# Kernel optimization log

Hardware: AMD Instinct MI355X
Metric: run time of the kernel (lower is better)

The kernel has to match this reference:

```python
import jax, jax.numpy as jnp
import numpy as np

EMB = 1024
HEADS = 16

def setup_inputs() -> dict:
    key = jax.random.key(0)
    ks = jax.random.split(key, 9)
    s = 1.0 / np.sqrt(EMB)
    x = jax.random.normal(ks[0], (2, 2048, EMB), dtype=jnp.float32)
    Wq = jax.random.normal(ks[1], (EMB, EMB), dtype=jnp.float32) * s
    bq = jax.random.normal(ks[2], (EMB,), dtype=jnp.float32) * s
    Wk = jax.random.normal(ks[3], (EMB, EMB), dtype=jnp.float32) * s
    bk = jax.random.normal(ks[4], (EMB,), dtype=jnp.float32) * s
    Wv = jax.random.normal(ks[5], (EMB, EMB), dtype=jnp.float32) * s
    bv = jax.random.normal(ks[6], (EMB,), dtype=jnp.float32) * s
    Wo = jax.random.normal(ks[7], (EMB, EMB), dtype=jnp.float32) * s
    bo = jax.random.normal(ks[8], (EMB,), dtype=jnp.float32) * s
    return {"x": x, "Wq": Wq, "bq": bq, "Wk": Wk, "bk": bk, "Wv": Wv, "bv": bv, "Wo": Wo, "bo": bo}

def reference(x, Wq, bq, Wk, bk, Wv, bv, Wo, bo):
    B, N, E = x.shape
    H = HEADS
    D = E // H
    # q/k/v projections, split heads: b n (h d) -> b h n d
    def proj(W, b):
        y = jnp.einsum('bne,ef->bnf', x, W.T) + b
        return y.reshape(B, N, H, D).transpose(0, 2, 1, 3)
    q = proj(Wq, bq)
    k = proj(Wk, bk)
    v = proj(Wv, bv)
    energy = jnp.einsum('bhqd,bhkd->bhqk', q, k)
    scaling = jnp.asarray(E, x.dtype) ** 0.5  # note: sqrt(emb_size), as in source
    att = jax.nn.softmax(energy / scaling, axis=-1)
    out = jnp.einsum('bhqk,bhkd->bhqd', att, v)
    out = out.transpose(0, 2, 1, 3).reshape(B, N, E)  # b h n d -> b n (h d)
    return jnp.einsum('bne,ef->bnf', out, Wo.T) + bo
```

## Files before the change

### kernel.cpp

```cpp
#include <hip/hip_runtime.h>
#include <hip/hip_bf16.h>
#include <stdint.h>

typedef __bf16 bf16;
typedef __bf16 bf16x8 __attribute__((ext_vector_type(8)));
typedef __bf16 bf16x4 __attribute__((ext_vector_type(4)));
typedef __bf16 bf16x2 __attribute__((ext_vector_type(2)));
typedef float  f32x4  __attribute__((ext_vector_type(4)));
typedef float  f32x16 __attribute__((ext_vector_type(16)));
typedef unsigned int uint;

#define MFMA(a,b,c)   __builtin_amdgcn_mfma_f32_16x16x32_bf16((a),(b),(c),0,0,0)
#define MFMA32(a,b,c) __builtin_amdgcn_mfma_f32_32x32x16_bf16((a),(b),(c),0,0,0)
#define EXP2(x)       __builtin_amdgcn_exp2f(x)

__device__ __forceinline__ void gload_lds16(const void* g, void* lds) {
  __builtin_amdgcn_global_load_lds(
      (const __attribute__((address_space(1))) uint32_t*)g,
      (__attribute__((address_space(3))) uint32_t*)lds, 16, 0, 0);
}

__device__ __forceinline__ uint pk_bf16(float lo, float hi) {
  bf16x2 v; v[0] = (bf16)lo; v[1] = (bf16)hi;
  return __builtin_bit_cast(uint, v);
}

__global__ __launch_bounds__(256) void k_cvt(
    const float* __restrict__ x,
    const float* __restrict__ wq, const float* __restrict__ wk,
    const float* __restrict__ wv, const float* __restrict__ wo,
    bf16* __restrict__ xb, bf16* __restrict__ wqb, bf16* __restrict__ wkb,
    bf16* __restrict__ wvb, bf16* __restrict__ wob)
{
  int r = blockIdx.y;
  const float* s; bf16* d; int n;
  switch (r) {
    case 0: s = x;  d = xb;  n = 4194304; break;
    case 1: s = wq; d = wqb; n = 1048576; break;
    case 2: s = wk; d = wkb; n = 1048576; break;
    case 3: s = wv; d = wvb; n = 1048576; break;
    default: s = wo; d = wob; n = 1048576; break;
  }
  int i = (blockIdx.x * 256 + threadIdx.x) * 8;
  if (i >= n) return;
  const float4* sp = (const float4*)(s + i);
  float4 a = sp[0], b = sp[1];
  bf16x8 o;
  o[0]=(bf16)a.x; o[1]=(bf16)a.y; o[2]=(bf16)a.z; o[3]=(bf16)a.w;
  o[4]=(bf16)b.x; o[5]=(bf16)b.y; o[6]=(bf16)b.z; o[7]=(bf16)b.w;
  *(bf16x8*)(d + i) = o;
}

__global__ __launch_bounds__(256, 2) void k_gemm_qkv(
    const bf16* __restrict__ A,
    const bf16* __restrict__ Wq, const bf16* __restrict__ Wk, const bf16* __restrict__ Wv,
    const float* __restrict__ bq, const float* __restrict__ bk, const float* __restrict__ bv,
    bf16* __restrict__ Qw, bf16* __restrict__ Kw, bf16* __restrict__ Vtw)
{
  __shared__ __align__(16) char As[2][8192];
  __shared__ __align__(16) char Bs[2][8192];
  int tid = threadIdx.x;
  int wv4 = tid >> 6, l = tid & 63, lo = l & 15, hi = l >> 4;
  int f = blockIdx.y * 32 + blockIdx.x;
  int xcd = f & 7, i8 = f >> 3;
  int mt = xcd * 4 + (i8 & 3);
  int ft = i8 >> 2;
  int wsel = ft >> 3;
  const bf16* W = (wsel == 0) ? Wq : (wsel == 1) ? Wk : Wv;
  const float* bias = (wsel == 0) ? bq : (wsel == 1) ? bk : bv;
  int f0 = (ft & 7) * 128;
  const bf16* Ab = A + (size_t)mt * 128 * 1024;
  const bf16* Wb = W + (size_t)f0 * 1024;
  const bf16* Pa = (wsel < 2) ? Wb : Ab;
  const bf16* Pb = (wsel < 2) ? Ab : Wb;
  int wm = wv4 >> 1, wf = wv4 & 1;
  f32x4 acc[4][4];
  #pragma unroll
  for (int i = 0; i < 4; i++)
    #pragma unroll
    for (int j = 0; j < 4; j++) acc[i][j] = (f32x4){0.f, 0.f, 0.f, 0.f};

  #define STAGEG(t, bi) {                                              \
    int k0 = (t) * 32;                                                 \
    _Pragma("unroll")                                                  \
    for (int p = 0; p < 2; p++) {                                      \
      int sp = p * 256 + tid;                                          \
      int row = sp >> 2, s = sp & 3;                                   \
      int gc = k0 + 8 * (s ^ ((row >> 1) & 3));                        \
      gload_lds16(Pa + (size_t)row * 1024 + gc, As[bi] + sp * 16);     \
      gload_lds16(Pb + (size_t)row * 1024 + gc, Bs[bi] + sp * 16);     \
    } }

  STAGEG(0, 0);
  for (int t = 0; t < 32; ++t) {
    __syncthreads();
    if (t < 31) STAGEG(t + 1, (t + 1) & 1);
    const char* Ac = As[t & 1];
    const char* Bc = Bs[t & 1];
    bf16x8 af[4], bfr[4];
    #pragma unroll
    for (int ms = 0; ms < 4; ms++) {
      int row = wm * 64 + ms * 16 + lo;
      af[ms] = *(const bf16x8*)(Ac + row * 64 + 16 * (hi ^ ((row >> 1) & 3)));
    }
    #pragma unroll
    for (int fs = 0; fs < 4; fs++) {
      int row = wf * 64 + fs * 16 + lo;
      bfr[fs] = *(const bf16x8*)(Bc + row * 64 + 16 * (hi ^ ((row >> 1) & 3)));
    }
    __builtin_amdgcn_s_setprio(1);
    #pragma unroll
    for (int ms = 0; ms < 4; ms++)
      #pragma unroll
      for (int fs = 0; fs < 4; fs++)
        acc[ms][fs] = MFMA(af[ms], bfr[fs], acc[ms][fs]);
    __builtin_amdgcn_s_setprio(0);
  }
  #undef STAGEG

  if (wsel < 2) {
    bf16* Outp = (wsel == 0) ? Qw : Kw;
    float qs = (wsel == 0) ? 0.0450842199527801f : 1.0f;
    #pragma unroll
    for (int ms = 0; ms < 4; ms++) {
      int fl = f0 + wm * 64 + ms * 16 + hi * 4;
      int h = fl >> 6, dd = fl & 63;
      float4 b4 = *(const float4*)(bias + fl);
      #pragma unroll
      for (int fs = 0; fs < 4; fs++) {
        int m = mt * 128 + wf * 64 + fs * 16 + lo;
        int b = m >> 11, nn = m & 2047;
        bf16x4 w;
        #pragma unroll
        for (int r = 0; r < 4; r++)
          w[r] = (bf16)((acc[ms][fs][r] + ((const float*)&b4)[r]) * qs);
        *(bf16x4*)(Outp + (((size_t)(b * 16 + h) * 2048 + nn) * 64) + dd) = w;
      }
    }
  } else {
    #pragma unroll
    for (int fs = 0; fs < 4; fs++) {
      int fl = f0 + wf * 64 + fs * 16 + lo;
      int h = fl >> 6, dd = fl & 63;
      float bb = bias[fl];
      #pragma unroll
      for (int ms = 0; ms < 4; ms++) {
        int m = mt * 128 + wm * 64 + ms * 16 + hi * 4;
        int b = m >> 11, nn = m & 2047;
        bf16x4 w;
        #pragma unroll
        for (int r = 0; r < 4; r++) w[r] = (bf16)(acc[ms][fs][r] + bb);
        *(bf16x4*)(Vtw + (((size_t)(b * 16 + h) * 64 + dd) * 2048) + nn) = w;
      }
    }
  }
}

__global__ __launch_bounds__(256, 2) void k_attn(
    const bf16* __restrict__ Q, const bf16* __restrict__ K,
    const bf16* __restrict__ Vt, bf16* __restrict__ O)
{
  __shared__ __align__(16) char Ks[3][8192];
  __shared__ __align__(16) char Vs[3][8192];
  int tid = threadIdx.x;
  int wid = tid >> 6, l = tid & 63;
  int lq = l & 31, hi1 = l >> 5;
  int f = blockIdx.y * 16 + blockIdx.x;
  int xcd = f & 7, i8 = f >> 3;
  int bh = xcd * 4 + (i8 & 3);
  int qt = i8 >> 2;
  int qg = qt * 128 + wid * 32 + lq;
  const bf16* Kb = K + (size_t)bh * 2048 * 64;
  const bf16* Vb = Vt + (size_t)bh * 64 * 2048;

  bf16x8 qf[4];
  const bf16* Qb = Q + ((size_t)bh * 2048 + qg) * 64 + hi1 * 8;
  #pragma unroll
  for (int c = 0; c < 4; c++) qf[c] = *(const bf16x8*)(Qb + 16 * c);

  f32x16 o0, o1, zz;
  #pragma unroll
  for (int r = 0; r < 16; r++) { zz[r] = 0.f; o0[r] = 0.f; o1[r] = 0.f; }
  float ls = 0.f;

  int srow = tid >> 3, slot = tid & 7;
  int swz = 16 * (slot ^ (srow & 7));
  int swk = lq & 7;
  uint4 k0r, k1r, v0r, v1r;
  #define STAGE(t) {                                                          \
    k0r = *(const uint4*)(Kb + (size_t)((t)*64 + srow) * 64 + slot * 8);      \
    k1r = *(const uint4*)(Kb + (size_t)((t)*64 + srow + 32) * 64 + slot * 8); \
    v0r = *(const uint4*)(Vb + (size_t)srow * 2048 + (t)*64 + slot * 8);      \
    v1r = *(const uint4*)(Vb + (size_t)(srow + 32) * 2048 + (t)*64 + slot * 8); }
  #define WRBUF(bi) {                                  \
    *(uint4*)(Ks[bi] + srow * 128 + swz)        = k0r; \
    *(uint4*)(Ks[bi] + (srow + 32) * 128 + swz) = k1r; \
    *(uint4*)(Vs[bi] + srow * 128 + swz)        = v0r; \
    *(uint4*)(Vs[bi] + (srow + 32) * 128 + swz) = v1r; }
  #define EXPSUM(S, T0, T1, T2, T3)                     \
    _Pragma("unroll")                                   \
    for (int r = 0; r < 16; r += 4) {                   \
      S[r]   = EXP2(S[r]);   T0 += S[r];                \
      S[r+1] = EXP2(S[r+1]); T1 += S[r+1];              \
      S[r+2] = EXP2(S[r+2]); T2 += S[r+2];              \
      S[r+3] = EXP2(S[r+3]); T3 += S[r+3];              \
    }
  #define PACK(dst, plo, phi)                                                \
    _Pragma("unroll")                                                        \
    for (int m = 0; m < 2; m++) {                                            \
      uint a0 = pk_bf16(plo[8*m+0], plo[8*m+1]);                             \
      uint b0 = pk_bf16(plo[8*m+4], plo[8*m+5]);                             \
      asm volatile("v_permlane32_swap_b32 %0, %1" : "+v"(a0), "+v"(b0));     \
      uint a1 = pk_bf16(plo[8*m+2], plo[8*m+3]);                             \
      uint b1 = pk_bf16(plo[8*m+6], plo[8*m+7]);                             \
      asm volatile("v_permlane32_swap_b32 %0, %1" : "+v"(a1), "+v"(b1));     \
      dst[m] = (uint4){a0, a1, b0, b1};                                      \
      uint c0 = pk_bf16(phi[8*m+0], phi[8*m+1]);                             \
      uint d0 = pk_bf16(phi[8*m+4], phi[8*m+5]);                             \
      asm volatile("v_permlane32_swap_b32 %0, %1" : "+v"(c0), "+v"(d0));     \
      uint c1 = pk_bf16(phi[8*m+2], phi[8*m+3]);                             \
      uint d1 = pk_bf16(phi[8*m+6], phi[8*m+7]);                             \
      asm volatile("v_permlane32_swap_b32 %0, %1" : "+v"(c1), "+v"(d1));     \
      dst[2+m] = (uint4){c0, c1, d0, d1};                                    \
    }
  #define QKT(bi, S0, S1) {                                                  \
    bf16x8 kf0[4], kf1[4];                                                   \
    _Pragma("unroll")                                                        \
    for (int c = 0; c < 4; c++) {                                            \
      kf0[c] = *(const bf16x8*)(Ks[bi] + lq * 128 + 16 * ((2*c + hi1) ^ swk));        \
      kf1[c] = *(const bf16x8*)(Ks[bi] + (32 + lq) * 128 + 16 * ((2*c + hi1) ^ swk)); \
    }                                                                        \
    __builtin_amdgcn_s_setprio(1);                                           \
    S0 = MFMA32(kf0[0], qf[0], zz);                                          \
    S1 = MFMA32(kf1[0], qf[0], zz);                                          \
    _Pragma("unroll")                                                        \
    for (int c = 1; c < 4; c++) {                                            \
      S0 = MFMA32(kf0[c], qf[c], S0);                                        \
      S1 = MFMA32(kf1[c], qf[c], S1);                                        \
    }                                                                        \
    __builtin_amdgcn_s_setprio(0); }
  #define SMPV(bi, S0, S1) {                                                 \
    float e0 = 0.f, e1 = 0.f, e2 = 0.f, e3 = 0.f;                            \
    EXPSUM(S0, e0, e1, e2, e3);                                              \
    EXPSUM(S1, e0, e1, e2, e3);                                              \
    ls += (e0 + e1) + (e2 + e3);                                             \
    uint4 pf[4];                                                             \
    PACK(pf, S0, S1);                                                        \
    __builtin_amdgcn_s_setprio(1);                                           \
    _Pragma("unroll")                                                        \
    for (int c = 0; c < 4; c++) {                                            \
      bf16x8 pb = __builtin_bit_cast(bf16x8, pf[c]);                         \
      bf16x8 vf0 = *(const bf16x8*)(Vs[bi] + lq * 128 + 16 * ((2*c + hi1) ^ swk));        \
      o0 = MFMA32(vf0, pb, o0);                                              \
      bf16x8 vf1 = *(const bf16x8*)(Vs[bi] + (32 + lq) * 128 + 16 * ((2*c + hi1) ^ swk)); \
      o1 = MFMA32(vf1, pb, o1);                                              \
    }                                                                        \
    __builtin_amdgcn_s_setprio(0); }
  #define BODY(t, SC0, SC1, SN0, SN1) {                                      \
    __syncthreads();                                                         \
    if ((t) < 31) QKT(((t) + 1) % 3, SN0, SN1);                              \
    if ((t) < 30) WRBUF(((t) + 2) % 3);                                      \
    SMPV((t) % 3, SC0, SC1);                                                 \
    if ((t) < 29) STAGE((t) + 3); }

  STAGE(0); WRBUF(0); STAGE(1);
  __syncthreads();
  WRBUF(1); STAGE(2);
  f32x16 sA0, sA1, sB0, sB1;
  QKT(0, sA0, sA1);

  for (int tt = 0; tt < 32; tt += 2) {
    BODY(tt,     sA0, sA1, sB0, sB1);
    BODY(tt + 1, sB0, sB1, sA0, sA1);
  }
  #undef STAGE
  #undef WRBUF
  #undef QKT
  #undef SMPV
  #undef BODY

  float lsum = ls + __shfl_xor(ls, 32);
  float inv = 1.0f / lsum;
  int b = bh >> 4, h = bh & 15;
  bf16* Ob = O + ((size_t)(b * 2048 + qg)) * 1024 + h * 64 + hi1 * 4;
  #pragma unroll
  for (int g = 0; g < 4; g++) {
    bf16x4 w0, w1;
    #pragma unroll
    for (int j = 0; j < 4; j++) {
      w0[j] = (bf16)(o0[4*g+j] * inv);
      w1[j] = (bf16)(o1[4*g+j] * inv);
    }
    *(bf16x4*)(Ob + g * 8)      = w0;
    *(bf16x4*)(Ob + 32 + g * 8) = w1;
  }
}

__global__ __launch_bounds__(512, 1) void k_gemm_out(
    const bf16* __restrict__ A,
    const bf16* __restrict__ W,
    const float* __restrict__ bias,
    float* __restrict__ Cout)
{
  __shared__ __align__(16) char As[2][16384];
  __shared__ __align__(16) char Bs[2][16384];
  int tid = threadIdx.x;
  int wid = tid >> 6, l = tid & 63, lo = l & 15, hi = l >> 4;
  int f = blockIdx.y * 32 + blockIdx.x;
  int xcd = f & 7, i8 = f >> 3;
  int mt = xcd * 4 + (i8 & 3);
  int f0 = (i8 >> 2) * 128;
  const bf16* Ab = A + (size_t)mt * 128 * 1024;
  const bf16* Wb = W + (size_t)f0 * 1024;
  int wm2 = wid >> 2, wf4 = wid & 3;
  f32x4 acc[2][4];
  #pragma unroll
  for (int i = 0; i < 2; i++)
    #pragma unroll
    for (int j = 0; j < 4; j++) acc[i][j] = (f32x4){0.f, 0.f, 0.f, 0.f};

  #define STAGEG(t, bi) {                                              \
    int k0 = (t) * 64;                                                 \
    _Pragma("unroll")                                                  \
    for (int p = 0; p < 2; p++) {                                      \
      int sp = p * 512 + tid;                                          \
      int row = sp >> 3, s = sp & 7;                                   \
      int gc = k0 + 8 * (s ^ (row & 7));                               \
      gload_lds16(Wb + (size_t)row * 1024 + gc, As[bi] + sp * 16);     \
      gload_lds16(Ab + (size_t)row * 1024 + gc, Bs[bi] + sp * 16);     \
    } }

  STAGEG(0, 0);
  for (int t = 0; t < 16; ++t) {
    __syncthreads();
    if (t < 15) STAGEG(t + 1, (t + 1) & 1);
    const char* Ac = As[t & 1];
    const char* Bc = Bs[t & 1];
    #pragma unroll
    for (int kk = 0; kk < 2; kk++) {
      bf16x8 wfr[2], afr[4];
      #pragma unroll
      for (int i = 0; i < 2; i++) {
        int row = wf4 * 32 + i * 16 + lo;
        wfr[i] = *(const bf16x8*)(Ac + row * 128 + 16 * ((kk * 4 + hi) ^ (row & 7)));
      }
      #pragma unroll
      for (int j = 0; j < 4; j++) {
        int row = wm2 * 64 + j * 16 + lo;
        afr[j] = *(const bf16x8*)(Bc + row * 128 + 16 * ((kk * 4 + hi) ^ (row & 7)));
      }
      __builtin_amdgcn_s_setprio(1);
      #pragma unroll
      for (int i = 0; i < 2; i++)
        #pragma unroll
        for (int j = 0; j < 4; j++)
          acc[i][j] = MFMA(wfr[i], afr[j], acc[i][j]);
      __builtin_amdgcn_s_setprio(0);
    }
  }
  #undef STAGEG

  #pragma unroll
  for (int i = 0; i < 2; i++) {
    int fl = f0 + wf4 * 32 + i * 16 + hi * 4;
    float4 b4 = *(const float4*)(bias + fl);
    #pragma unroll
    for (int j = 0; j < 4; j++) {
      int m = mt * 128 + wm2 * 64 + j * 16 + lo;
      float4 o;
      o.x = acc[i][j][0] + b4.x;
      o.y = acc[i][j][1] + b4.y;
      o.z = acc[i][j][2] + b4.z;
      o.w = acc[i][j][3] + b4.w;
      *(float4*)(Cout + (size_t)m * 1024 + fl) = o;
    }
  }
}

extern "C" void kernel_launch(void* const* d_in, const int* in_sizes, int n_in,
                              void* d_out, int out_size, void* d_ws, size_t ws_size,
                              hipStream_t stream) {
  const float* x  = (const float*)d_in[0];
  const float* Wq = (const float*)d_in[1];
  const float* bq = (const float*)d_in[2];
  const float* Wk = (const float*)d_in[3];
  const float* bk = (const float*)d_in[4];
  const float* Wv = (const float*)d_in[5];
  const float* bv = (const float*)d_in[6];
  const float* Wo = (const float*)d_in[7];
  const float* bo = (const float*)d_in[8];
  float* out = (float*)d_out;
  char* ws = (char*)d_ws;

  bf16* xb  = (bf16*)(ws);
  bf16* wqb = (bf16*)(ws + 8388608);
  bf16* wkb = (bf16*)(ws + 10485760);
  bf16* wvb = (bf16*)(ws + 12582912);
  bf16* wob = (bf16*)(ws + 14680064);
  bf16* Qw  = (bf16*)(ws + 16777216);
  bf16* Kw  = (bf16*)(ws + 25165824);
  bf16* Vtw = (bf16*)(ws + 33554432);
  bf16* Ow  = (bf16*)(ws + 41943040);

  k_cvt<<<dim3(2048, 5), 256, 0, stream>>>(x, Wq, Wk, Wv, Wo, xb, wqb, wkb, wvb, wob);
  k_gemm_qkv<<<dim3(32, 24), 256, 0, stream>>>(xb, wqb, wkb, wvb, bq, bk, bv, Qw, Kw, Vtw);
  k_attn<<<dim3(16, 32), 256, 0, stream>>>(Qw, Kw, Vtw, Ow);
  k_gemm_out<<<dim3(32, 8), 512, 0, stream>>>(Ow, wob, bo, out);
}
```

Measured before the change: 108.8 us.

## Restructure attention KV pipeline into two-tile epochs with four LDS buffers

Changes the attention kernel's K/V pipeline from a 3-buffer, one-tile-per-barrier schedule to a 4-buffer schedule that processes two KV tiles per __syncthreads. Register staging is doubled so two tiles are prefetched at once. The aim is to halve the number of block barriers and issue global loads further ahead. The cost is that QK^T and softmax·V for each tile now run back-to-back without cross-tile overlap inside an epoch. LDS use also grows from 48KB to 64KB and more staging registers are held, which may limit occupancy at 2 blocks per CU.

```diff
diff --git a/kernel.cpp b/kernel.cpp
--- a/kernel.cpp
+++ b/kernel.cpp
@@ -160,8 +160,8 @@
     const bf16* __restrict__ Q, const bf16* __restrict__ K,
     const bf16* __restrict__ Vt, bf16* __restrict__ O)
 {
-  __shared__ __align__(16) char Ks[3][8192];
-  __shared__ __align__(16) char Vs[3][8192];
+  __shared__ __align__(16) char Ks[4][8192];
+  __shared__ __align__(16) char Vs[4][8192];
   int tid = threadIdx.x;
   int wid = tid >> 6, l = tid & 63;
   int lq = l & 31, hi1 = l >> 5;
@@ -186,17 +186,28 @@
   int srow = tid >> 3, slot = tid & 7;
   int swz = 16 * (slot ^ (srow & 7));
   int swk = lq & 7;
-  uint4 k0r, k1r, v0r, v1r;
-  #define STAGE(t) {                                                          \
-    k0r = *(const uint4*)(Kb + (size_t)((t)*64 + srow) * 64 + slot * 8);      \
-    k1r = *(const uint4*)(Kb + (size_t)((t)*64 + srow + 32) * 64 + slot * 8); \
-    v0r = *(const uint4*)(Vb + (size_t)srow * 2048 + (t)*64 + slot * 8);      \
-    v1r = *(const uint4*)(Vb + (size_t)(srow + 32) * 2048 + (t)*64 + slot * 8); }
-  #define WRBUF(bi) {                                  \
-    *(uint4*)(Ks[bi] + srow * 128 + swz)        = k0r; \
-    *(uint4*)(Ks[bi] + (srow + 32) * 128 + swz) = k1r; \
-    *(uint4*)(Vs[bi] + srow * 128 + swz)        = v0r; \
-    *(uint4*)(Vs[bi] + (srow + 32) * 128 + swz) = v1r; }
+  uint4 xk0, xk1, xv0, xv1;
+  uint4 yk0, yk1, yv0, yv1;
+  #define STAGEX(t) {                                                          \
+    xk0 = *(const uint4*)(Kb + (size_t)((t)*64 + srow) * 64 + slot * 8);       \
+    xk1 = *(const uint4*)(Kb + (size_t)((t)*64 + srow + 32) * 64 + slot * 8);  \
+    xv0 = *(const uint4*)(Vb + (size_t)srow * 2048 + (t)*64 + slot * 8);       \
+    xv1 = *(const uint4*)(Vb + (size_t)(srow + 32) * 2048 + (t)*64 + slot * 8); }
+  #define STAGEY(t) {                                                          \
+    yk0 = *(const uint4*)(Kb + (size_t)((t)*64 + srow) * 64 + slot * 8);       \
+    yk1 = *(const uint4*)(Kb + (size_t)((t)*64 + srow + 32) * 64 + slot * 8);  \
+    yv0 = *(const uint4*)(Vb + (size_t)srow * 2048 + (t)*64 + slot * 8);       \
+    yv1 = *(const uint4*)(Vb + (size_t)(srow + 32) * 2048 + (t)*64 + slot * 8); }
+  #define WRX(bi) {                                     \
+    *(uint4*)(Ks[bi] + srow * 128 + swz)        = xk0;  \
+    *(uint4*)(Ks[bi] + (srow + 32) * 128 + swz) = xk1;  \
+    *(uint4*)(Vs[bi] + srow * 128 + swz)        = xv0;  \
+    *(uint4*)(Vs[bi] + (srow + 32) * 128 + swz) = xv1; }
+  #define WRY(bi) {                                     \
+    *(uint4*)(Ks[bi] + srow * 128 + swz)        = yk0;  \
+    *(uint4*)(Ks[bi] + (srow + 32) * 128 + swz) = yk1;  \
+    *(uint4*)(Vs[bi] + srow * 128 + swz)        = yv0;  \
+    *(uint4*)(Vs[bi] + (srow + 32) * 128 + swz) = yv1; }
   #define EXPSUM(S, T0, T1, T2, T3)                     \
     _Pragma("unroll")                                   \
     for (int r = 0; r < 16; r += 4) {                   \
@@ -256,28 +267,32 @@
       o1 = MFMA32(vf1, pb, o1);                                              \
     }                                                                        \
     __builtin_amdgcn_s_setprio(0); }
-  #define BODY(t, SC0, SC1, SN0, SN1) {                                      \
+  #define EPOCH(TT, B0, B1, B2, B3) {                                        \
     __syncthreads();                                                         \
-    if ((t) < 31) QKT(((t) + 1) % 3, SN0, SN1);                              \
-    if ((t) < 30) WRBUF(((t) + 2) % 3);                                      \
-    SMPV((t) % 3, SC0, SC1);                                                 \
-    if ((t) < 29) STAGE((t) + 3); }
-
-  STAGE(0); WRBUF(0); STAGE(1);
-  __syncthreads();
-  WRBUF(1); STAGE(2);
-  f32x16 sA0, sA1, sB0, sB1;
-  QKT(0, sA0, sA1);
-
-  for (int tt = 0; tt < 32; tt += 2) {
-    BODY(tt,     sA0, sA1, sB0, sB1);
-    BODY(tt + 1, sB0, sB1, sA0, sA1);
-  }
-  #undef STAGE
-  #undef WRBUF
+    f32x16 sA0, sA1, sB0, sB1;                                               \
+    QKT(B0, sA0, sA1);                                                       \
+    if ((TT) < 30) WRX(B2);                                                  \
+    SMPV(B0, sA0, sA1);                                                      \
+    QKT(B1, sB0, sB1);                                                       \
+    if ((TT) < 30) WRY(B3);                                                  \
+    SMPV(B1, sB0, sB1);                                                      \
+    if ((TT) < 28) { STAGEX((TT) + 4); STAGEY((TT) + 5); } }
+
+  STAGEX(0); STAGEY(1);
+  WRX(0); WRY(1);
+  STAGEX(2); STAGEY(3);
+
+  for (int tt = 0; tt < 32; tt += 4) {
+    EPOCH(tt,     0, 1, 2, 3);
+    EPOCH(tt + 2, 2, 3, 0, 1);
+  }
+  #undef STAGEX
+  #undef STAGEY
+  #undef WRX
+  #undef WRY
   #undef QKT
   #undef SMPV
-  #undef BODY
+  #undef EPOCH
 
   float lsum = ls + __shfl_xor(ls, 32);
   float inv = 1.0f / lsum;
```

Result: faster. 105.6 us (-3.0%).
